# Performance work log

Hardware: AMD Instinct MI355X
Metric: run time of the kernel (lower is better)

## Reference

```python
import jax, jax.numpy as jnp
import numpy as np

N = 50000   # nodes
E = 800000  # edges
D = 64      # feature dim
C = 1.0     # curvature
MIN_NORM = 1e-15
BALL_EPS = 4e-3  # float32 projection epsilon (hgcn convention)


def _artanh(x):
    x = jnp.clip(x, -1.0 + 1e-7, 1.0 - 1e-7)
    return jnp.arctanh(x)


def _norm(x):
    return jnp.maximum(jnp.linalg.norm(x, axis=-1, keepdims=True), MIN_NORM)


def expmap0(u, c):
    # euclidean2poincare: tangent at origin -> ball
    sqrt_c = jnp.sqrt(c)
    u_norm = _norm(u)
    return jnp.tanh(sqrt_c * u_norm) * u / (sqrt_c * u_norm)


def logmap0(p, c):
    # poincare2euclidean: ball -> tangent at origin
    sqrt_c = jnp.sqrt(c)
    p_norm = _norm(p)
    return _artanh(sqrt_c * p_norm) * p / (sqrt_c * p_norm)


def proj(x, c):
    sqrt_c = jnp.sqrt(c)
    norm = _norm(x)
    maxnorm = (1.0 - BALL_EPS) / sqrt_c
    return jnp.where(norm > maxnorm, x / norm * maxnorm, x)


def mobius_matvec(m, x, c):
    # m: [out, in], x: [N, in]
    sqrt_c = jnp.sqrt(c)
    x_norm = _norm(x)                      # [N,1]
    mx = x @ m.T                           # [N,out]
    mx_norm = _norm(mx)                    # [N,1]
    res = jnp.tanh(mx_norm / x_norm * _artanh(sqrt_c * x_norm)) * mx / (mx_norm * sqrt_c)
    zero_mask = jnp.all(mx == 0.0, axis=-1, keepdims=True)
    return jnp.where(zero_mask, jnp.zeros_like(res), res)


def setup_inputs() -> dict:
    key = jax.random.key(0)
    k1, k2, k3, k4 = jax.random.split(key, 4)
    # node features: small norm so points lie well inside the unit ball
    x = jax.random.normal(k1, (N, D), dtype=jnp.float32) * 0.05
    # xavier_uniform-ish scale for the weight
    W = jax.random.normal(k2, (D, D), dtype=jnp.float32) * np.float32(np.sqrt(2.0 / D))
    edge_index = jax.random.randint(k3, (2, E), 0, N)
    edge_weight = jax.random.uniform(k4, (E,), dtype=jnp.float32)
    return {"x": x, "W": W, "edge_weight": edge_weight, "edge_index": edge_index}


def reference(x, W, edge_weight, edge_index):
    c = jnp.float32(C)
    # Linear (dropout=0, no bias): mobius matvec in the ball
    hidden = mobius_matvec(W, x, c)                       # [N,D] in ball
    # poincare2euclidean
    hidden_e = logmap0(hidden, c)                         # [N,D]
    # sparse adjacency aggregation: support = A @ hidden_e
    row, col = edge_index[0], edge_index[1]
    msgs = edge_weight[:, None] * hidden_e[col]           # [E,D]
    support = jax.ops.segment_sum(msgs, row, num_segments=N)  # [N,D]
    # euclidean2poincare
    support = expmap0(support, c)
    # HypAct: logmap0(c_in) -> relu -> expmap0(c_out) -> proj
    xt = jax.nn.relu(logmap0(support, c))
    out = proj(expmap0(xt, c), c)
    return out
```

## Files before the change

### kernel.cpp

```cpp
#include <hip/hip_runtime.h>
#include <hip/hip_bf16.h>
#include <math.h>

#define DD 64
#define BROWS 64
#define BSH 6
#define MAXB 1024
#define CAPB 1536
#define BINB 512
#define BINC 3072
#define LROWS 128
typedef unsigned long long u64;
typedef unsigned int u32;
typedef unsigned short u16;
typedef __fp16 f16x2 __attribute__((ext_vector_type(2)));

__global__ __launch_bounds__(1024) void hgcn_zero0(int* __restrict__ bcur,
                                                   int* __restrict__ nspill) {
  const int i = threadIdx.x;
  if (i < MAXB) bcur[i] = 0;
  if (i == 0) nspill[0] = 0;
}

__global__ __launch_bounds__(512) void hgcn_linbin(const float* __restrict__ x,
                                                   const float* __restrict__ W,
                                                   __hip_bfloat16* __restrict__ he,
                                                   const int* __restrict__ ei,
                                                   const float* __restrict__ ew,
                                                   int* __restrict__ bcur,
                                                   u64* __restrict__ stage,
                                                   u64* __restrict__ spill,
                                                   int* __restrict__ nspill,
                                                   int n, int ne, int nbin) {
  const int tid = threadIdx.x;
  if ((int)blockIdx.x < nbin) {
    __shared__ int h[MAXB], gp[MAXB];
    h[tid] = 0; h[tid + 512] = 0;
    __syncthreads();
    const int eb = blockIdx.x * BINC;
    const int m = min(BINC, ne - eb);
    int r[6], c[6], rk[6];
    float w[6];
    int cnt = 0;
    #pragma unroll
    for (int k = 0; k < 6; ++k) {
      const int i = tid + k * BINB;
      if (i < m) {
        r[k] = ei[eb + i];
        c[k] = ei[ne + eb + i];
        w[k] = ew[eb + i];
        rk[k] = atomicAdd(&h[r[k] >> BSH], 1);
        cnt = k + 1;
      }
    }
    __syncthreads();
    {
      const int v0 = h[tid];
      gp[tid] = v0 ? atomicAdd(&bcur[tid], v0) : 0;
      const int v1 = h[tid + 512];
      gp[tid + 512] = v1 ? atomicAdd(&bcur[tid + 512], v1) : 0;
    }
    __syncthreads();
    for (int k = 0; k < cnt; ++k) {
      const int b = r[k] >> BSH;
      const int pos = gp[b] + rk[k];
      if (pos < CAPB) {
        stage[(size_t)b * CAPB + pos] =
            ((u64)__float_as_uint(w[k]) << 32) | ((u32)(r[k] & (BROWS - 1)) << 16) | (u32)c[k];
      } else {
        const int sp = atomicAdd(nspill, 1);
        spill[sp] = ((u64)__float_as_uint(w[k]) << 32) | ((u32)(r[k] & 0xffff) << 16) | (u32)c[k];
      }
    }
  } else {
    __shared__ f16x2 xsh[8][32];
    const int lb = (int)blockIdx.x - nbin;
    const int wave = tid >> 6, lane = tid & 63;
    f16x2 Wh[32];
    #pragma unroll
    for (int m4 = 0; m4 < 16; ++m4) {
      const float4 wv = *reinterpret_cast<const float4*>(W + lane * 64 + m4 * 4);
      Wh[2 * m4]     = __builtin_amdgcn_cvt_pkrtz(wv.x, wv.y);
      Wh[2 * m4 + 1] = __builtin_amdgcn_cvt_pkrtz(wv.z, wv.w);
    }
    const int rbase = lb * LROWS + wave * 16;
    for (int q = 0; q < 16; ++q) {
      const int row = rbase + q;
      if (row >= n) break;
      const float xv = x[(size_t)row * DD + lane];
      float nx2 = xv * xv;
      #pragma unroll
      for (int mm = 1; mm < 64; mm <<= 1) nx2 += __shfl_xor(nx2, mm);
      const float nx = fmaxf(sqrtf(nx2), 1e-15f);
      const float z  = fminf(nx, 1.f - 1e-7f);
      const float s  = 0.5f * __logf((1.f + z) / (1.f - z)) / nx;
      const float xo = __shfl_xor(xv, 1);
      if (!(lane & 1)) xsh[wave][lane >> 1] = __builtin_amdgcn_cvt_pkrtz(xv, xo);
      float acc = 0.f;
      #pragma unroll
      for (int m2 = 0; m2 < 32; ++m2)
        acc = __builtin_amdgcn_fdot2(xsh[wave][m2], Wh[m2], acc, false);
      he[(size_t)row * DD + lane] = __float2bfloat16(acc * s);
    }
  }
}

__global__ __launch_bounds__(1024) void hgcn_bagg(const u16* __restrict__ he,
                                                  const u64* __restrict__ stage,
                                                  const int* __restrict__ bcur,
                                                  const u64* __restrict__ spill,
                                                  const int* __restrict__ nspill,
                                                  float* __restrict__ out, int n) {
  __shared__ u64 edr[CAPB];
  __shared__ u64 ed[CAPB];
  __shared__ int lh[BROWS + 1];
  __shared__ int lcur[BROWS];
  const int t = threadIdx.x;
  const int b = blockIdx.x;
  const u64* sb = stage + (size_t)b * CAPB;
  const int cnt = min(bcur[b], CAPB);

  for (int i = t; i < cnt; i += 1024) edr[i] = sb[i];
  if (t < BROWS) lcur[t] = 0;
  __syncthreads();
  for (int i = t; i < cnt; i += 1024)
    atomicAdd(&lcur[(int)((edr[i] >> 16) & (BROWS - 1))], 1);
  __syncthreads();
  if (t < 64) {
    const int v = lcur[t];
    int sc = v;
    #pragma unroll
    for (int d = 1; d < 64; d <<= 1) {
      const int u2 = __shfl_up(sc, d);
      if (t >= d) sc += u2;
    }
    lh[t] = sc - v;
    lcur[t] = sc - v;
    if (t == 63) lh[64] = sc;
  }
  __syncthreads();
  for (int i = t; i < cnt; i += 1024) {
    const u64 p = edr[i];
    const int rl = (int)((p >> 16) & (BROWS - 1));
    const int pos = atomicAdd(&lcur[rl], 1);
    ed[pos] = p;
  }
  __syncthreads();

  const int row = t >> 4;
  const int u = t & 15;
  const int s = u >> 3;
  const int l = u & 7;
  float a[8] = {0.f, 0.f, 0.f, 0.f, 0.f, 0.f, 0.f, 0.f};

  int j = lh[row] + s;
  const int je = lh[row + 1];
  uint4 q = {0, 0, 0, 0};
  float w = 0.f;
  if (j < je) {
    const u64 p = ed[j];
    w = __uint_as_float((u32)(p >> 32));
    q = reinterpret_cast<const uint4*>(he + ((size_t)(p & 0xffffu) << 6))[l];
  }
  while (j < je) {
    const uint4 qc = q;
    const float wc = w;
    const int jn = j + 2;
    if (jn < je) {
      const u64 p = ed[jn];
      w = __uint_as_float((u32)(p >> 32));
      q = reinterpret_cast<const uint4*>(he + ((size_t)(p & 0xffffu) << 6))[l];
    }
    a[0] = fmaf(wc, __uint_as_float(qc.x << 16), a[0]);
    a[1] = fmaf(wc, __uint_as_float(qc.x & 0xffff0000u), a[1]);
    a[2] = fmaf(wc, __uint_as_float(qc.y << 16), a[2]);
    a[3] = fmaf(wc, __uint_as_float(qc.y & 0xffff0000u), a[3]);
    a[4] = fmaf(wc, __uint_as_float(qc.z << 16), a[4]);
    a[5] = fmaf(wc, __uint_as_float(qc.z & 0xffff0000u), a[5]);
    a[6] = fmaf(wc, __uint_as_float(qc.w << 16), a[6]);
    a[7] = fmaf(wc, __uint_as_float(qc.w & 0xffff0000u), a[7]);
    j = jn;
  }

  const int ns = nspill[0];
  for (int sidx = 0; sidx < ns; ++sidx) {
    const u64 p = spill[sidx];
    const int grow = (int)((p >> 16) & 0xffffu);
    if ((grow >> BSH) != b) continue;
    if ((grow & (BROWS - 1)) != row || s != 0) continue;
    const float ww = __uint_as_float((u32)(p >> 32));
    const uint4 qq = reinterpret_cast<const uint4*>(he + ((size_t)(p & 0xffffu) << 6))[l];
    a[0] = fmaf(ww, __uint_as_float(qq.x << 16), a[0]);
    a[1] = fmaf(ww, __uint_as_float(qq.x & 0xffff0000u), a[1]);
    a[2] = fmaf(ww, __uint_as_float(qq.y << 16), a[2]);
    a[3] = fmaf(ww, __uint_as_float(qq.y & 0xffff0000u), a[3]);
    a[4] = fmaf(ww, __uint_as_float(qq.z << 16), a[4]);
    a[5] = fmaf(ww, __uint_as_float(qq.z & 0xffff0000u), a[5]);
    a[6] = fmaf(ww, __uint_as_float(qq.w << 16), a[6]);
    a[7] = fmaf(ww, __uint_as_float(qq.w & 0xffff0000u), a[7]);
  }

  #pragma unroll
  for (int k = 0; k < 8; ++k) a[k] += __shfl_xor(a[k], 8);

  float ss = 0.f;
  #pragma unroll
  for (int k = 0; k < 8; ++k) { a[k] = fmaxf(a[k], 0.f); ss = fmaf(a[k], a[k], ss); }
  ss += __shfl_xor(ss, 1); ss += __shfl_xor(ss, 2); ss += __shfl_xor(ss, 4);
  const float nu = fmaxf(sqrtf(ss), 1e-15f);
  const float th = tanhf(nu);
  const float maxn = 1.0f - 4e-3f;
  const float scale = (th > maxn) ? (maxn / nu) : (th / nu);
  const int grow = (b << BSH) + row;
  if (s == 0 && grow < n) {
    float4* op = reinterpret_cast<float4*>(out + (size_t)grow * DD + (size_t)l * 8);
    op[0] = float4{a[0] * scale, a[1] * scale, a[2] * scale, a[3] * scale};
    op[1] = float4{a[4] * scale, a[5] * scale, a[6] * scale, a[7] * scale};
  }
}

__global__ __launch_bounds__(256) void hgcn_linf32(const float* __restrict__ x,
                                                   const float* __restrict__ W,
                                                   float* __restrict__ he, int n) {
  __shared__ float Wl[64][68];
  __shared__ float xs[4][64];
  const int tid = threadIdx.x;
  for (int i = tid; i < 64 * 64; i += 256) Wl[i >> 6][i & 63] = W[i];
  const int wave = tid >> 6, lane = tid & 63;
  const int row = blockIdx.x * 4 + wave;
  float xv = 0.f;
  if (row < n) xv = x[row * DD + lane];
  xs[wave][lane] = xv;
  __syncthreads();
  if (row >= n) return;
  float nx2 = xv * xv;
  #pragma unroll
  for (int m = 1; m < 64; m <<= 1) nx2 += __shfl_xor(nx2, m);
  const float nx = fmaxf(sqrtf(nx2), 1e-15f);
  const float s = atanhf(fminf(nx, 1.f - 1e-7f)) / nx;
  const int j0 = (lane >> 3) & 7;
  float acc = 0.f;
  #pragma unroll
  for (int jj = 0; jj < 16; ++jj) {
    const int k = ((jj + j0) & 15) << 2;
    const float4 xk = *reinterpret_cast<const float4*>(&xs[wave][k]);
    const float4 wk = *reinterpret_cast<const float4*>(&Wl[lane][k]);
    acc = fmaf(xk.x, wk.x, acc); acc = fmaf(xk.y, wk.y, acc);
    acc = fmaf(xk.z, wk.z, acc); acc = fmaf(xk.w, wk.w, acc);
  }
  he[row * DD + lane] = acc * s;
}

__global__ __launch_bounds__(256) void hgcn_zero(float* __restrict__ p, int n4) {
  const int i = blockIdx.x * 256 + threadIdx.x;
  if (i < n4) reinterpret_cast<float4*>(p)[i] = float4{0.f, 0.f, 0.f, 0.f};
}

__global__ __launch_bounds__(256) void hgcn_scatter(const float* __restrict__ he,
                                                    const int* __restrict__ ei,
                                                    const float* __restrict__ ew,
                                                    float* __restrict__ sup, int ne) {
  const int t = blockIdx.x * 256 + threadIdx.x;
  const int e = t >> 4, l = t & 15;
  if (e >= ne) return;
  const int row = ei[e];
  const int col = ei[ne + e];
  const float w = ew[e];
  const float4 v = *reinterpret_cast<const float4*>(he + (size_t)col * DD + l * 4);
  float* dst = sup + (size_t)row * DD + l * 4;
  unsafeAtomicAdd(dst + 0, w * v.x);
  unsafeAtomicAdd(dst + 1, w * v.y);
  unsafeAtomicAdd(dst + 2, w * v.z);
  unsafeAtomicAdd(dst + 3, w * v.w);
}

__global__ __launch_bounds__(256) void hgcn_final(const float* __restrict__ sup,
                                                  float* __restrict__ out, int n) {
  const int t = blockIdx.x * 256 + threadIdx.x;
  const int r = t >> 4, l = t & 15;
  if (r >= n) return;
  float4 v = *reinterpret_cast<const float4*>(sup + (size_t)r * DD + l * 4);
  v.x = fmaxf(v.x, 0.f); v.y = fmaxf(v.y, 0.f);
  v.z = fmaxf(v.z, 0.f); v.w = fmaxf(v.w, 0.f);
  float p = v.x*v.x + v.y*v.y + v.z*v.z + v.w*v.w;
  p += __shfl_xor(p, 1); p += __shfl_xor(p, 2);
  p += __shfl_xor(p, 4); p += __shfl_xor(p, 8);
  const float nu = fmaxf(sqrtf(p), 1e-15f);
  const float th = tanhf(nu);
  float scale = th / nu;
  const float maxn = 1.0f - 4e-3f;
  if (th > maxn) scale = maxn / nu;
  float4 o = {v.x*scale, v.y*scale, v.z*scale, v.w*scale};
  *reinterpret_cast<float4*>(out + (size_t)r * DD + l * 4) = o;
}

extern "C" void kernel_launch(void* const* d_in, const int* in_sizes, int n_in,
                              void* d_out, int out_size, void* d_ws, size_t ws_size,
                              hipStream_t stream) {
  const float* x  = (const float*)d_in[0];
  const float* W  = (const float*)d_in[1];
  const float* ew = (const float*)d_in[2];
  const int*   ei = (const int*)d_in[3];
  const int n  = in_sizes[0] / DD;
  const int ne = in_sizes[2];
  const int nb = (n + BROWS - 1) / BROWS;

  size_t off_he    = 0;
  size_t off_stage = off_he + (((size_t)n * DD * 2 + 15) / 16) * 16;
  size_t off_spill = off_stage + (size_t)MAXB * CAPB * 8;
  size_t off_bcur  = off_spill + (size_t)ne * 8;
  size_t off_nsp   = off_bcur + MAXB * 4;
  size_t need      = off_nsp + 64;

  const size_t mean = (size_t)ne / (size_t)nb;
  size_t sig = 1;
  while (sig * sig < mean) ++sig;
  const bool capOK = mean + 8 * sig <= CAPB;

  if (ws_size >= need && n <= 65535 && nb <= MAXB && capOK) {
    __hip_bfloat16* he = (__hip_bfloat16*)((char*)d_ws + off_he);
    u64* stage  = (u64*)((char*)d_ws + off_stage);
    u64* spill  = (u64*)((char*)d_ws + off_spill);
    int* bcur   = (int*)((char*)d_ws + off_bcur);
    int* nspill = (int*)((char*)d_ws + off_nsp);
    float* out  = (float*)d_out;

    const int nbin = (ne + BINC - 1) / BINC;
    const int nlin = (n + LROWS - 1) / LROWS;

    hipLaunchKernelGGL(hgcn_zero0,  dim3(1),           dim3(1024), 0, stream, bcur, nspill);
    hipLaunchKernelGGL(hgcn_linbin, dim3(nbin + nlin), dim3(512),  0, stream,
                       x, W, he, ei, ew, bcur, stage, spill, nspill, n, ne, nbin);
    hipLaunchKernelGGL(hgcn_bagg,   dim3(nb),          dim3(1024), 0, stream,
                       (const u16*)he, stage, bcur, spill, nspill, out, n);
  } else {
    float* he  = (float*)d_out;
    float* sup = (float*)d_ws;
    float* out = (float*)d_out;
    const int n4 = n * DD / 4;
    hipLaunchKernelGGL(hgcn_zero,    dim3((n4 + 255) / 256),       dim3(256), 0, stream, sup, n4);
    hipLaunchKernelGGL(hgcn_linf32,  dim3((n + 3) / 4),            dim3(256), 0, stream, x, W, he, n);
    hipLaunchKernelGGL(hgcn_scatter, dim3((ne * 16 + 255) / 256),  dim3(256), 0, stream, he, ei, ew, sup, ne);
    hipLaunchKernelGGL(hgcn_final,   dim3((n * 16 + 255) / 256),   dim3(256), 0, stream, sup, out, n);
  }
}
```

Measured before the change: 60.98 us.

## Fuse zero, bin/linear, and aggregate stages into one cooperative persistent kernel

Replaces three kernel launches with one cooperative kernel. It uses grid-wide syncs between the zeroing, the binning/linear phase and the aggregation phase, and its blocks loop persistently over work items. The aggregation now runs on 512 threads, one half-row group per row instead of two strided lanes per row. This removes launch gaps and the cross-kernel tail. In exchange it adds grid.sync overhead, a fixed grid of at most 512 blocks, and one block processing several buckets one after another. The grid size assumes 256 CUs, and each block now holds a larger shared memory footprint, which could lower occupancy.

Measured after the change: 199.8 us. 228% more time.

```diff
diff --git a/kernel.cpp b/kernel.cpp
--- a/kernel.cpp
+++ b/kernel.cpp
@@ -1,13 +1,15 @@
 #include <hip/hip_runtime.h>
+#include <hip/hip_cooperative_groups.h>
 #include <hip/hip_bf16.h>
 #include <math.h>
+
+namespace cg = cooperative_groups;
 
 #define DD 64
 #define BROWS 64
 #define BSH 6
 #define MAXB 1024
 #define CAPB 1536
-#define BINB 512
 #define BINC 3072
 #define LROWS 128
 typedef unsigned long long u64;
@@ -15,207 +17,201 @@
 typedef unsigned short u16;
 typedef __fp16 f16x2 __attribute__((ext_vector_type(2)));
 
-__global__ __launch_bounds__(1024) void hgcn_zero0(int* __restrict__ bcur,
-                                                   int* __restrict__ nspill) {
-  const int i = threadIdx.x;
-  if (i < MAXB) bcur[i] = 0;
-  if (i == 0) nspill[0] = 0;
-}
-
-__global__ __launch_bounds__(512) void hgcn_linbin(const float* __restrict__ x,
-                                                   const float* __restrict__ W,
-                                                   __hip_bfloat16* __restrict__ he,
-                                                   const int* __restrict__ ei,
-                                                   const float* __restrict__ ew,
-                                                   int* __restrict__ bcur,
-                                                   u64* __restrict__ stage,
-                                                   u64* __restrict__ spill,
-                                                   int* __restrict__ nspill,
-                                                   int n, int ne, int nbin) {
+__global__ __launch_bounds__(512) void hgcn_coop(const float* __restrict__ x,
+                                                 const float* __restrict__ W,
+                                                 __hip_bfloat16* __restrict__ he,
+                                                 const int* __restrict__ ei,
+                                                 const float* __restrict__ ew,
+                                                 int* __restrict__ bcur,
+                                                 u64* __restrict__ stage,
+                                                 u64* __restrict__ spill,
+                                                 int* __restrict__ nspill,
+                                                 float* __restrict__ out,
+                                                 int n, int ne, int nbin, int nlinc, int nb) {
+  cg::grid_group grid = cg::this_grid();
   const int tid = threadIdx.x;
-  if ((int)blockIdx.x < nbin) {
-    __shared__ int h[MAXB], gp[MAXB];
-    h[tid] = 0; h[tid + 512] = 0;
-    __syncthreads();
-    const int eb = blockIdx.x * BINC;
-    const int m = min(BINC, ne - eb);
-    int r[6], c[6], rk[6];
-    float w[6];
-    int cnt = 0;
-    #pragma unroll
-    for (int k = 0; k < 6; ++k) {
-      const int i = tid + k * BINB;
-      if (i < m) {
-        r[k] = ei[eb + i];
-        c[k] = ei[ne + eb + i];
-        w[k] = ew[eb + i];
-        rk[k] = atomicAdd(&h[r[k] >> BSH], 1);
-        cnt = k + 1;
-      }
-    }
-    __syncthreads();
-    {
-      const int v0 = h[tid];
-      gp[tid] = v0 ? atomicAdd(&bcur[tid], v0) : 0;
-      const int v1 = h[tid + 512];
-      gp[tid + 512] = v1 ? atomicAdd(&bcur[tid + 512], v1) : 0;
-    }
-    __syncthreads();
-    for (int k = 0; k < cnt; ++k) {
-      const int b = r[k] >> BSH;
-      const int pos = gp[b] + rk[k];
-      if (pos < CAPB) {
-        stage[(size_t)b * CAPB + pos] =
-            ((u64)__float_as_uint(w[k]) << 32) | ((u32)(r[k] & (BROWS - 1)) << 16) | (u32)c[k];
-      } else {
-        const int sp = atomicAdd(nspill, 1);
-        spill[sp] = ((u64)__float_as_uint(w[k]) << 32) | ((u32)(r[k] & 0xffff) << 16) | (u32)c[k];
-      }
-    }
-  } else {
-    __shared__ f16x2 xsh[8][32];
-    const int lb = (int)blockIdx.x - nbin;
-    const int wave = tid >> 6, lane = tid & 63;
-    f16x2 Wh[32];
-    #pragma unroll
-    for (int m4 = 0; m4 < 16; ++m4) {
-      const float4 wv = *reinterpret_cast<const float4*>(W + lane * 64 + m4 * 4);
-      Wh[2 * m4]     = __builtin_amdgcn_cvt_pkrtz(wv.x, wv.y);
-      Wh[2 * m4 + 1] = __builtin_amdgcn_cvt_pkrtz(wv.z, wv.w);
-    }
-    const int rbase = lb * LROWS + wave * 16;
-    for (int q = 0; q < 16; ++q) {
-      const int row = rbase + q;
-      if (row >= n) break;
-      const float xv = x[(size_t)row * DD + lane];
-      float nx2 = xv * xv;
+  const int G = gridDim.x;
+  __shared__ int h[MAXB], gp[MAXB];
+  __shared__ u64 edr[CAPB], ed[CAPB];
+  __shared__ f16x2 xsh[8][32];
+  __shared__ int lh[BROWS + 1], lcur[BROWS];
+
+  for (int i = blockIdx.x * 512 + tid; i < MAXB + 1; i += G * 512) {
+    if (i < MAXB) bcur[i] = 0;
+    else nspill[0] = 0;
+  }
+  grid.sync();
+
+  for (int wi = blockIdx.x; wi < nbin + nlinc; wi += G) {
+    if (wi < nbin) {
+      __syncthreads();
+      h[tid] = 0; h[tid + 512] = 0;
+      __syncthreads();
+      const int eb = wi * BINC;
+      const int m = min(BINC, ne - eb);
+      int r[6], c[6], rk[6];
+      float w[6];
+      int cnt2 = 0;
       #pragma unroll
-      for (int mm = 1; mm < 64; mm <<= 1) nx2 += __shfl_xor(nx2, mm);
-      const float nx = fmaxf(sqrtf(nx2), 1e-15f);
-      const float z  = fminf(nx, 1.f - 1e-7f);
-      const float s  = 0.5f * __logf((1.f + z) / (1.f - z)) / nx;
-      const float xo = __shfl_xor(xv, 1);
-      if (!(lane & 1)) xsh[wave][lane >> 1] = __builtin_amdgcn_cvt_pkrtz(xv, xo);
-      float acc = 0.f;
+      for (int k = 0; k < 6; ++k) {
+        const int i = tid + k * 512;
+        if (i < m) {
+          r[k] = ei[eb + i];
+          c[k] = ei[ne + eb + i];
+          w[k] = ew[eb + i];
+          rk[k] = atomicAdd(&h[r[k] >> BSH], 1);
+          cnt2 = k + 1;
+        }
+      }
+      __syncthreads();
+      {
+        const int v0 = h[tid];
+        gp[tid] = v0 ? atomicAdd(&bcur[tid], v0) : 0;
+        const int v1 = h[tid + 512];
+        gp[tid + 512] = v1 ? atomicAdd(&bcur[tid + 512], v1) : 0;
+      }
+      __syncthreads();
+      for (int k = 0; k < cnt2; ++k) {
+        const int b = r[k] >> BSH;
+        const int pos = gp[b] + rk[k];
+        if (pos < CAPB) {
+          stage[(size_t)b * CAPB + pos] =
+              ((u64)__float_as_uint(w[k]) << 32) | ((u32)(r[k] & (BROWS - 1)) << 16) | (u32)c[k];
+        } else {
+          const int sp = atomicAdd(nspill, 1);
+          spill[sp] = ((u64)__float_as_uint(w[k]) << 32) | ((u32)(r[k] & 0xffff) << 16) | (u32)c[k];
+        }
+      }
+    } else {
+      const int lb = wi - nbin;
+      const int wave = tid >> 6, lane = tid & 63;
+      f16x2 Wh[32];
       #pragma unroll
-      for (int m2 = 0; m2 < 32; ++m2)
-        acc = __builtin_amdgcn_fdot2(xsh[wave][m2], Wh[m2], acc, false);
-      he[(size_t)row * DD + lane] = __float2bfloat16(acc * s);
-    }
-  }
-}
-
-__global__ __launch_bounds__(1024) void hgcn_bagg(const u16* __restrict__ he,
-                                                  const u64* __restrict__ stage,
-                                                  const int* __restrict__ bcur,
-                                                  const u64* __restrict__ spill,
-                                                  const int* __restrict__ nspill,
-                                                  float* __restrict__ out, int n) {
-  __shared__ u64 edr[CAPB];
-  __shared__ u64 ed[CAPB];
-  __shared__ int lh[BROWS + 1];
-  __shared__ int lcur[BROWS];
-  const int t = threadIdx.x;
-  const int b = blockIdx.x;
-  const u64* sb = stage + (size_t)b * CAPB;
-  const int cnt = min(bcur[b], CAPB);
-
-  for (int i = t; i < cnt; i += 1024) edr[i] = sb[i];
-  if (t < BROWS) lcur[t] = 0;
-  __syncthreads();
-  for (int i = t; i < cnt; i += 1024)
-    atomicAdd(&lcur[(int)((edr[i] >> 16) & (BROWS - 1))], 1);
-  __syncthreads();
-  if (t < 64) {
-    const int v = lcur[t];
-    int sc = v;
-    #pragma unroll
-    for (int d = 1; d < 64; d <<= 1) {
-      const int u2 = __shfl_up(sc, d);
-      if (t >= d) sc += u2;
-    }
-    lh[t] = sc - v;
-    lcur[t] = sc - v;
-    if (t == 63) lh[64] = sc;
-  }
-  __syncthreads();
-  for (int i = t; i < cnt; i += 1024) {
-    const u64 p = edr[i];
-    const int rl = (int)((p >> 16) & (BROWS - 1));
-    const int pos = atomicAdd(&lcur[rl], 1);
-    ed[pos] = p;
-  }
-  __syncthreads();
-
-  const int row = t >> 4;
-  const int u = t & 15;
-  const int s = u >> 3;
-  const int l = u & 7;
-  float a[8] = {0.f, 0.f, 0.f, 0.f, 0.f, 0.f, 0.f, 0.f};
-
-  int j = lh[row] + s;
-  const int je = lh[row + 1];
-  uint4 q = {0, 0, 0, 0};
-  float w = 0.f;
-  if (j < je) {
-    const u64 p = ed[j];
-    w = __uint_as_float((u32)(p >> 32));
-    q = reinterpret_cast<const uint4*>(he + ((size_t)(p & 0xffffu) << 6))[l];
-  }
-  while (j < je) {
-    const uint4 qc = q;
-    const float wc = w;
-    const int jn = j + 2;
-    if (jn < je) {
-      const u64 p = ed[jn];
+      for (int m4 = 0; m4 < 16; ++m4) {
+        const float4 wv = *reinterpret_cast<const float4*>(W + lane * 64 + m4 * 4);
+        Wh[2 * m4]     = __builtin_amdgcn_cvt_pkrtz(wv.x, wv.y);
+        Wh[2 * m4 + 1] = __builtin_amdgcn_cvt_pkrtz(wv.z, wv.w);
+      }
+      const int rbase = lb * LROWS + wave * 16;
+      for (int q = 0; q < 16; ++q) {
+        const int row = rbase + q;
+        if (row >= n) break;
+        const float xv = x[(size_t)row * DD + lane];
+        float nx2 = xv * xv;
+        #pragma unroll
+        for (int mm = 1; mm < 64; mm <<= 1) nx2 += __shfl_xor(nx2, mm);
+        const float nx = fmaxf(sqrtf(nx2), 1e-15f);
+        const float z  = fminf(nx, 1.f - 1e-7f);
+        const float s  = 0.5f * __logf((1.f + z) / (1.f - z)) / nx;
+        const float xo = __shfl_xor(xv, 1);
+        if (!(lane & 1)) xsh[wave][lane >> 1] = __builtin_amdgcn_cvt_pkrtz(xv, xo);
+        float acc = 0.f;
+        #pragma unroll
+        for (int m2 = 0; m2 < 32; ++m2)
+          acc = __builtin_amdgcn_fdot2(xsh[wave][m2], Wh[m2], acc, false);
+        he[(size_t)row * DD + lane] = __float2bfloat16(acc * s);
+      }
+    }
+  }
+  __threadfence();
+  grid.sync();
+
+  const int ns = nspill[0];
+  for (int b = blockIdx.x; b < nb; b += G) {
+    __syncthreads();
+    const u64* sb = stage + (size_t)b * CAPB;
+    const int cnt = min(bcur[b], CAPB);
+    for (int i = tid; i < cnt; i += 512) edr[i] = sb[i];
+    if (tid < BROWS) lcur[tid] = 0;
+    __syncthreads();
+    for (int i = tid; i < cnt; i += 512)
+      atomicAdd(&lcur[(int)((edr[i] >> 16) & (BROWS - 1))], 1);
+    __syncthreads();
+    if (tid < 64) {
+      const int v = lcur[tid];
+      int sc = v;
+      #pragma unroll
+      for (int d = 1; d < 64; d <<= 1) {
+        const int u2 = __shfl_up(sc, d);
+        if (tid >= d) sc += u2;
+      }
+      lh[tid] = sc - v;
+      lcur[tid] = sc - v;
+      if (tid == 63) lh[64] = sc;
+    }
+    __syncthreads();
+    for (int i = tid; i < cnt; i += 512) {
+      const u64 p = edr[i];
+      const int rl = (int)((p >> 16) & (BROWS - 1));
+      const int pos = atomicAdd(&lcur[rl], 1);
+      ed[pos] = p;
+    }
+    __syncthreads();
+
+    const int row = tid >> 3;
+    const int l = tid & 7;
+    float a[8] = {0.f, 0.f, 0.f, 0.f, 0.f, 0.f, 0.f, 0.f};
+
+    int j = lh[row];
+    const int je = lh[row + 1];
+    uint4 q = {0, 0, 0, 0};
+    float w = 0.f;
+    if (j < je) {
+      const u64 p = ed[j];
       w = __uint_as_float((u32)(p >> 32));
       q = reinterpret_cast<const uint4*>(he + ((size_t)(p & 0xffffu) << 6))[l];
     }
-    a[0] = fmaf(wc, __uint_as_float(qc.x << 16), a[0]);
-    a[1] = fmaf(wc, __uint_as_float(qc.x & 0xffff0000u), a[1]);
-    a[2] = fmaf(wc, __uint_as_float(qc.y << 16), a[2]);
-    a[3] = fmaf(wc, __uint_as_float(qc.y & 0xffff0000u), a[3]);
-    a[4] = fmaf(wc, __uint_as_float(qc.z << 16), a[4]);
-    a[5] = fmaf(wc, __uint_as_float(qc.z & 0xffff0000u), a[5]);
-    a[6] = fmaf(wc, __uint_as_float(qc.w << 16), a[6]);
-    a[7] = fmaf(wc, __uint_as_float(qc.w & 0xffff0000u), a[7]);
-    j = jn;
-  }
-
-  const int ns = nspill[0];
-  for (int sidx = 0; sidx < ns; ++sidx) {
-    const u64 p = spill[sidx];
-    const int grow = (int)((p >> 16) & 0xffffu);
-    if ((grow >> BSH) != b) continue;
-    if ((grow & (BROWS - 1)) != row || s != 0) continue;
-    const float ww = __uint_as_float((u32)(p >> 32));
-    const uint4 qq = reinterpret_cast<const uint4*>(he + ((size_t)(p & 0xffffu) << 6))[l];
-    a[0] = fmaf(ww, __uint_as_float(qq.x << 16), a[0]);
-    a[1] = fmaf(ww, __uint_as_float(qq.x & 0xffff0000u), a[1]);
-    a[2] = fmaf(ww, __uint_as_float(qq.y << 16), a[2]);
-    a[3] = fmaf(ww, __uint_as_float(qq.y & 0xffff0000u), a[3]);
-    a[4] = fmaf(ww, __uint_as_float(qq.z << 16), a[4]);
-    a[5] = fmaf(ww, __uint_as_float(qq.z & 0xffff0000u), a[5]);
-    a[6] = fmaf(ww, __uint_as_float(qq.w << 16), a[6]);
-    a[7] = fmaf(ww, __uint_as_float(qq.w & 0xffff0000u), a[7]);
-  }
-
-  #pragma unroll
-  for (int k = 0; k < 8; ++k) a[k] += __shfl_xor(a[k], 8);
-
-  float ss = 0.f;
-  #pragma unroll
-  for (int k = 0; k < 8; ++k) { a[k] = fmaxf(a[k], 0.f); ss = fmaf(a[k], a[k], ss); }
-  ss += __shfl_xor(ss, 1); ss += __shfl_xor(ss, 2); ss += __shfl_xor(ss, 4);
-  const float nu = fmaxf(sqrtf(ss), 1e-15f);
-  const float th = tanhf(nu);
-  const float maxn = 1.0f - 4e-3f;
-  const float scale = (th > maxn) ? (maxn / nu) : (th / nu);
-  const int grow = (b << BSH) + row;
-  if (s == 0 && grow < n) {
-    float4* op = reinterpret_cast<float4*>(out + (size_t)grow * DD + (size_t)l * 8);
-    op[0] = float4{a[0] * scale, a[1] * scale, a[2] * scale, a[3] * scale};
-    op[1] = float4{a[4] * scale, a[5] * scale, a[6] * scale, a[7] * scale};
+    while (j < je) {
+      const uint4 qc = q;
+      const float wc = w;
+      const int jn = j + 1;
+      if (jn < je) {
+        const u64 p = ed[jn];
+        w = __uint_as_float((u32)(p >> 32));
+        q = reinterpret_cast<const uint4*>(he + ((size_t)(p & 0xffffu) << 6))[l];
+      }
+      a[0] = fmaf(wc, __uint_as_float(qc.x << 16), a[0]);
+      a[1] = fmaf(wc, __uint_as_float(qc.x & 0xffff0000u), a[1]);
+      a[2] = fmaf(wc, __uint_as_float(qc.y << 16), a[2]);
+      a[3] = fmaf(wc, __uint_as_float(qc.y & 0xffff0000u), a[3]);
+      a[4] = fmaf(wc, __uint_as_float(qc.z << 16), a[4]);
+      a[5] = fmaf(wc, __uint_as_float(qc.z & 0xffff0000u), a[5]);
+      a[6] = fmaf(wc, __uint_as_float(qc.w << 16), a[6]);
+      a[7] = fmaf(wc, __uint_as_float(qc.w & 0xffff0000u), a[7]);
+      j = jn;
+    }
+
+    for (int sidx = 0; sidx < ns; ++sidx) {
+      const u64 p = spill[sidx];
+      const int grow = (int)((p >> 16) & 0xffffu);
+      if ((grow >> BSH) != b) continue;
+      if ((grow & (BROWS - 1)) != row) continue;
+      const float ww = __uint_as_float((u32)(p >> 32));
+      const uint4 qq = reinterpret_cast<const uint4*>(he + ((size_t)(p & 0xffffu) << 6))[l];
+      a[0] = fmaf(ww, __uint_as_float(qq.x << 16), a[0]);
+      a[1] = fmaf(ww, __uint_as_float(qq.x & 0xffff0000u), a[1]);
+      a[2] = fmaf(ww, __uint_as_float(qq.y << 16), a[2]);
+      a[3] = fmaf(ww, __uint_as_float(qq.y & 0xffff0000u), a[3]);
+      a[4] = fmaf(ww, __uint_as_float(qq.z << 16), a[4]);
+      a[5] = fmaf(ww, __uint_as_float(qq.z & 0xffff0000u), a[5]);
+      a[6] = fmaf(ww, __uint_as_float(qq.w << 16), a[6]);
+      a[7] = fmaf(ww, __uint_as_float(qq.w & 0xffff0000u), a[7]);
+    }
+
+    float ss = 0.f;
+    #pragma unroll
+    for (int k = 0; k < 8; ++k) { a[k] = fmaxf(a[k], 0.f); ss = fmaf(a[k], a[k], ss); }
+    ss += __shfl_xor(ss, 1); ss += __shfl_xor(ss, 2); ss += __shfl_xor(ss, 4);
+    const float nu = fmaxf(sqrtf(ss), 1e-15f);
+    const float th = tanhf(nu);
+    const float maxn = 1.0f - 4e-3f;
+    const float scale = (th > maxn) ? (maxn / nu) : (th / nu);
+    const int grow = (b << BSH) + row;
+    if (grow < n) {
+      float4* op = reinterpret_cast<float4*>(out + (size_t)grow * DD + (size_t)l * 8);
+      op[0] = float4{a[0] * scale, a[1] * scale, a[2] * scale, a[3] * scale};
+      op[1] = float4{a[4] * scale, a[5] * scale, a[6] * scale, a[7] * scale};
+    }
   }
 }
 
@@ -317,7 +313,11 @@
   while (sig * sig < mean) ++sig;
   const bool capOK = mean + 8 * sig <= CAPB;
 
-  if (ws_size >= need && n <= 65535 && nb <= MAXB && capOK) {
+  int occ = 0;
+  hipError_t qerr = hipOccupancyMaxActiveBlocksPerMultiprocessor(&occ, hgcn_coop, 512, 0);
+  const bool coopOK = (qerr == hipSuccess && occ >= 1);
+
+  if (ws_size >= need && n <= 65535 && nb <= MAXB && capOK && coopOK) {
     __hip_bfloat16* he = (__hip_bfloat16*)((char*)d_ws + off_he);
     u64* stage  = (u64*)((char*)d_ws + off_stage);
     u64* spill  = (u64*)((char*)d_ws + off_spill);
@@ -325,14 +325,16 @@
     int* nspill = (int*)((char*)d_ws + off_nsp);
     float* out  = (float*)d_out;
 
-    const int nbin = (ne + BINC - 1) / BINC;
-    const int nlin = (n + LROWS - 1) / LROWS;
-
-    hipLaunchKernelGGL(hgcn_zero0,  dim3(1),           dim3(1024), 0, stream, bcur, nspill);
-    hipLaunchKernelGGL(hgcn_linbin, dim3(nbin + nlin), dim3(512),  0, stream,
-                       x, W, he, ei, ew, bcur, stage, spill, nspill, n, ne, nbin);
-    hipLaunchKernelGGL(hgcn_bagg,   dim3(nb),          dim3(1024), 0, stream,
-                       (const u16*)he, stage, bcur, spill, nspill, out, n);
+    int nbin  = (ne + BINC - 1) / BINC;
+    int nlinc = (n + LROWS - 1) / LROWS;
+    int G = occ * 256;
+    if (G > 512) G = 512;
+
+    void* args[] = {(void*)&x, (void*)&W, (void*)&he, (void*)&ei, (void*)&ew,
+                    (void*)&bcur, (void*)&stage, (void*)&spill, (void*)&nspill,
+                    (void*)&out, (void*)&n, (void*)&ne, (void*)&nbin, (void*)&nlinc,
+                    (void*)&nb};
+    hipLaunchCooperativeKernel((void*)hgcn_coop, dim3(G), dim3(512), args, 0, stream);
   } else {
     float* he  = (float*)d_out;
     float* sup = (float*)d_ws;
```
